# Optimization experiments

Hardware: AMD Instinct MI355X
Metric: run time of the kernel (lower is better)

The kernel has to match this reference:

```python
import jax, jax.numpy as jnp
import numpy as np

B, Q, K, D = 8, 2048, 2048, 512

def setup_inputs() -> dict:
    key = jax.random.key(0)
    k1, k2, k3, k4, k5 = jax.random.split(key, 5)
    return {
        "query": jax.random.normal(k1, (B, Q, D), dtype=jnp.float32),
        "key": jax.random.normal(k2, (B, K, D), dtype=jnp.float32),
        "value": jax.random.normal(k3, (B, K, D), dtype=jnp.float32),
        "key_mask": jax.random.randint(k4, (B, K), 0, 2, dtype=jnp.int32),
        "W": jax.random.normal(k5, (D, D), dtype=jnp.float32) / np.sqrt(D),
    }

def reference(query, key, value, key_mask, W):
    # bilinear score: s[b,q,k] = query[b,q,:] @ W @ key[b,k,:]
    scale = 1.0 / jnp.sqrt(jnp.asarray(query.shape[-1], query.dtype))
    qW = jnp.einsum('bqd,de->bqe', query, W)          # [B,Q,D]
    scores = jnp.einsum('bqe,bke->bqk', qW, key)      # [B,Q,K]
    scores = jnp.where(key_mask[:, None, :] == 0, jnp.asarray(-1e20, scores.dtype), scores) * scale
    dist = jax.nn.softmax(scores, axis=-1)            # [B,Q,K]
    context = jnp.einsum('bqk,bkd->bqd', dist, value) # [B,Q,D]
    return context, dist
```

## Files before the change

### kernel.cpp

```cpp
#include <hip/hip_runtime.h>
#include <stdint.h>

#define BB 8
#define QQ 2048
#define KK 2048
#define DD 512

typedef _Float16 f16x8 __attribute__((ext_vector_type(8)));
typedef float f32x4 __attribute__((ext_vector_type(4)));

__device__ __forceinline__ unsigned short f2h(float f) {
    union { _Float16 h; unsigned short u; } x;
    x.h = (_Float16)f;
    return x.u;
}
__device__ __forceinline__ float h2f(unsigned short u) {
    union { unsigned short u; _Float16 h; } x;
    x.u = u;
    return (float)x.h;
}

__device__ __forceinline__ void async16(const unsigned short* g, unsigned short* l) {
    __builtin_amdgcn_global_load_lds(
        (const __attribute__((address_space(1))) unsigned int*)g,
        (__attribute__((address_space(3))) unsigned int*)l, 16, 0, 0);
}

__global__ __launch_bounds__(256) void cvt_f32_f16_2(const float* __restrict__ in0,
                                                     const float* __restrict__ in1,
                                                     unsigned short* __restrict__ out0,
                                                     unsigned short* __restrict__ out1) {
    const float* in = blockIdx.y ? in1 : in0;
    unsigned short* out = blockIdx.y ? out1 : out0;
    size_t i = ((size_t)blockIdx.x * 256 + threadIdx.x) * 8;
    float4 a = *(const float4*)(in + i);
    float4 b = *(const float4*)(in + i + 4);
    uint4 u;
    u.x = (unsigned)f2h(a.x) | ((unsigned)f2h(a.y) << 16);
    u.y = (unsigned)f2h(a.z) | ((unsigned)f2h(a.w) << 16);
    u.z = (unsigned)f2h(b.x) | ((unsigned)f2h(b.y) << 16);
    u.w = (unsigned)f2h(b.z) | ((unsigned)f2h(b.w) << 16);
    *(uint4*)(out + i) = u;
}

__global__ __launch_bounds__(256) void transpose_cvt(const float* __restrict__ in,
                                                     unsigned short* __restrict__ out,
                                                     int R, int C, long inB, long outB) {
    __shared__ float t[32][33];
    const float* ip = in + (size_t)blockIdx.z * inB;
    unsigned short* op = out + (size_t)blockIdx.z * outB;
    int x = threadIdx.x & 31, y0 = threadIdx.x >> 5;
    int c0 = blockIdx.x * 32, r0 = blockIdx.y * 32;
#pragma unroll
    for (int i = 0; i < 32; i += 8)
        t[y0 + i][x] = ip[(size_t)(r0 + y0 + i) * C + c0 + x];
    __syncthreads();
#pragma unroll
    for (int i = 0; i < 32; i += 8)
        op[(size_t)(c0 + y0 + i) * R + r0 + x] = f2h(t[x][y0 + i]);
}

template <int OUTM>
__global__ __launch_bounds__(512, 2) void gemm256n(
    const unsigned short* __restrict__ Aall, const unsigned short* __restrict__ Ball,
    void* __restrict__ Call, const float* __restrict__ sums,
    int Kred, int lda, int ldb, int ldc,
    long aStride, long bStride, long cStride) {
    const int gx = gridDim.x, gy = gridDim.y;
    const int nwg = gx * gy * (int)gridDim.z;
    const int p = ((int)blockIdx.z * gy + (int)blockIdx.y) * gx + (int)blockIdx.x;
    const int qch = nwg >> 3, rch = nwg & 7;
    const int xcd = p & 7, ooff = p >> 3;
    const int w = (xcd < rch ? xcd * (qch + 1) : rch * (qch + 1) + (xcd - rch) * qch) + ooff;
    const int b = w / (gx * gy);
    const int rem = w - b * (gx * gy);
    const int my = rem / gx;
    const int nx = rem - my * gx;
    const int m0 = my * 256;
    const int n0 = nx * 128;

    __shared__ unsigned short As[4][256 * 32];
    __shared__ unsigned short Bs[4][128 * 32];

    const int tid = threadIdx.x;
    const int lane = tid & 63, wv = tid >> 6;
    const int wm = wv >> 2, wn = wv & 3;
    const int lrow = lane & 15, quad = lane >> 4;

    const int sr = lane >> 2;
    const int ssl = (lane & 3) ^ ((sr >> 1) & 3);
    const unsigned short* Ab = Aall + (size_t)b * aStride + (size_t)m0 * lda;
    const unsigned short* Bb = Ball + (size_t)b * bStride + (size_t)n0 * ldb;

    const int NT = Kred >> 5;

    auto stageA = [&](int t) {
#pragma unroll
        for (int j = 0; j < 2; j++) {
            const int c = wv * 2 + j;
            const int r = c * 16 + sr;
            async16(Ab + (size_t)r * lda + t * 32 + ssl * 8, &As[t & 3][c * 512]);
        }
    };
    auto stageB = [&](int t) {
        const int c = wv;
        const int r = c * 16 + sr;
        async16(Bb + (size_t)r * ldb + t * 32 + ssl * 8, &Bs[t & 3][c * 512]);
    };

    f32x4 acc[8][2];
#pragma unroll
    for (int mi = 0; mi < 8; mi++)
#pragma unroll
        for (int ni = 0; ni < 2; ni++)
            acc[mi][ni] = (f32x4){0.f, 0.f, 0.f, 0.f};

    for (int tt = 0; tt < 3 && tt < NT; ++tt) { stageA(tt); stageB(tt); }

    const int rsw = (lrow >> 1) & 3;

    for (int t = 0; t < NT; ++t) {
        if (t + 2 < NT)      asm volatile("s_waitcnt vmcnt(6)" ::: "memory");
        else if (t + 1 < NT) asm volatile("s_waitcnt vmcnt(3)" ::: "memory");
        else                 asm volatile("s_waitcnt vmcnt(0)" ::: "memory");
        __builtin_amdgcn_s_barrier();
        __builtin_amdgcn_sched_barrier(0);

        const unsigned short* Asl = As[t & 3];
        const unsigned short* Bsl = Bs[t & 3];
        f16x8 af[4], bfr[2];

        if (t + 3 < NT) stageA(t + 3);
#pragma unroll
        for (int ni = 0; ni < 2; ni++)
            bfr[ni] = *(const f16x8*)&Bsl[(wn * 32 + ni * 16 + lrow) * 32 + ((quad ^ rsw) * 8)];
#pragma unroll
        for (int mi = 0; mi < 4; mi++)
            af[mi] = *(const f16x8*)&Asl[(wm * 128 + mi * 16 + lrow) * 32 + ((quad ^ rsw) * 8)];
        __builtin_amdgcn_s_setprio(1);
#pragma unroll
        for (int mi = 0; mi < 4; mi++)
#pragma unroll
            for (int ni = 0; ni < 2; ni++)
                acc[mi][ni] = __builtin_amdgcn_mfma_f32_16x16x32_f16(af[mi], bfr[ni],
                                                                     acc[mi][ni], 0, 0, 0);
        __builtin_amdgcn_s_setprio(0);

        if (t + 3 < NT) stageB(t + 3);
#pragma unroll
        for (int mi = 0; mi < 4; mi++)
            af[mi] = *(const f16x8*)&Asl[(wm * 128 + (mi + 4) * 16 + lrow) * 32 + ((quad ^ rsw) * 8)];
        __builtin_amdgcn_s_setprio(1);
#pragma unroll
        for (int mi = 0; mi < 4; mi++)
#pragma unroll
            for (int ni = 0; ni < 2; ni++)
                acc[mi + 4][ni] = __builtin_amdgcn_mfma_f32_16x16x32_f16(af[mi], bfr[ni],
                                                                         acc[mi + 4][ni], 0, 0, 0);
        __builtin_amdgcn_s_setprio(0);
    }

#pragma unroll
    for (int mi = 0; mi < 8; mi++) {
        const int gm = m0 + wm * 128 + mi * 16 + quad * 4;
        if constexpr (OUTM == 0) {
            unsigned short* C = (unsigned short*)Call + (size_t)b * cStride;
#pragma unroll
            for (int ni = 0; ni < 2; ni++) {
                int gn = n0 + wn * 32 + ni * 16 + lrow;
#pragma unroll
                for (int r = 0; r < 4; r++)
                    C[(size_t)(gm + r) * ldc + gn] = f2h(acc[mi][ni][r]);
            }
        } else {
            float* C = (float*)Call + (size_t)b * cStride;
            const float* s = sums + (size_t)b * QQ;
            float iv[4];
#pragma unroll
            for (int r = 0; r < 4; r++) iv[r] = 1.0f / s[gm + r];
#pragma unroll
            for (int ni = 0; ni < 2; ni++) {
                int gn = n0 + wn * 32 + ni * 16 + lrow;
#pragma unroll
                for (int r = 0; r < 4; r++)
                    C[(size_t)(gm + r) * ldc + gn] = acc[mi][ni][r] * iv[r];
            }
        }
    }
}

__global__ __launch_bounds__(512, 2) void gemm256_exp(
    const unsigned short* __restrict__ Aall, const unsigned short* __restrict__ Ball,
    unsigned short* __restrict__ Call, const int* __restrict__ maskAll,
    float* __restrict__ sums, int Kred, int lda, int ldb, int ldc,
    long aStride, long bStride, long cStride, int maskStride, float scale) {
    const int gx = gridDim.x, gy = gridDim.y;
    const int nwg = gx * gy * (int)gridDim.z;
    const int p = ((int)blockIdx.z * gy + (int)blockIdx.y) * gx + (int)blockIdx.x;
    const int qch = nwg >> 3, rch = nwg & 7;
    const int xcd = p & 7, ooff = p >> 3;
    const int w = (xcd < rch ? xcd * (qch + 1) : rch * (qch + 1) + (xcd - rch) * qch) + ooff;
    const int b = w / (gx * gy);
    const int rem = w - b * (gx * gy);
    const int my = rem / gx;
    const int nx = rem - my * gx;
    const int m0 = my * 256;
    const int n0 = nx * 256;

    __shared__ unsigned short As[4][256 * 32];
    __shared__ unsigned short Bs[4][256 * 32];

    const int tid = threadIdx.x;
    const int lane = tid & 63, wv = tid >> 6;
    const int wm = wv >> 2, wn = wv & 3;
    const int lrow = lane & 15, quad = lane >> 4;

    const int sr = lane >> 2;
    const int ssl = (lane & 3) ^ ((sr >> 1) & 3);
    const unsigned short* Ab = Aall + (size_t)b * aStride + (size_t)m0 * lda;
    const unsigned short* Bb = Ball + (size_t)b * bStride + (size_t)n0 * ldb;

    const int NT = Kred >> 5;

    auto stageA = [&](int t) {
#pragma unroll
        for (int j = 0; j < 2; j++) {
            const int c = wv * 2 + j;
            const int r = c * 16 + sr;
            async16(Ab + (size_t)r * lda + t * 32 + ssl * 8, &As[t & 3][c * 512]);
        }
    };
    auto stageB = [&](int t) {
#pragma unroll
        for (int j = 0; j < 2; j++) {
            const int c = wv * 2 + j;
            const int r = c * 16 + sr;
            async16(Bb + (size_t)r * ldb + t * 32 + ssl * 8, &Bs[t & 3][c * 512]);
        }
    };

    f32x4 acc[8][4];
#pragma unroll
    for (int mi = 0; mi < 8; mi++)
#pragma unroll
        for (int ni = 0; ni < 4; ni++)
            acc[mi][ni] = (f32x4){0.f, 0.f, 0.f, 0.f};

    for (int tt = 0; tt < 3 && tt < NT; ++tt) { stageA(tt); stageB(tt); }

    const int rsw = (lrow >> 1) & 3;

    for (int t = 0; t < NT; ++t) {
        if (t + 2 < NT)      asm volatile("s_waitcnt vmcnt(8)" ::: "memory");
        else if (t + 1 < NT) asm volatile("s_waitcnt vmcnt(4)" ::: "memory");
        else                 asm volatile("s_waitcnt vmcnt(0)" ::: "memory");
        __builtin_amdgcn_s_barrier();
        __builtin_amdgcn_sched_barrier(0);

        const unsigned short* Asl = As[t & 3];
        const unsigned short* Bsl = Bs[t & 3];
        f16x8 af[4], bfr[4];

        if (t + 3 < NT) stageA(t + 3);
#pragma unroll
        for (int ni = 0; ni < 4; ni++)
            bfr[ni] = *(const f16x8*)&Bsl[(wn * 64 + ni * 16 + lrow) * 32 + ((quad ^ rsw) * 8)];
#pragma unroll
        for (int mi = 0; mi < 4; mi++)
            af[mi] = *(const f16x8*)&Asl[(wm * 128 + mi * 16 + lrow) * 32 + ((quad ^ rsw) * 8)];
        __builtin_amdgcn_s_setprio(1);
#pragma unroll
        for (int mi = 0; mi < 4; mi++)
#pragma unroll
            for (int ni = 0; ni < 4; ni++)
                acc[mi][ni] = __builtin_amdgcn_mfma_f32_16x16x32_f16(af[mi], bfr[ni],
                                                                     acc[mi][ni], 0, 0, 0);
        __builtin_amdgcn_s_setprio(0);

        if (t + 3 < NT) stageB(t + 3);
#pragma unroll
        for (int mi = 0; mi < 4; mi++)
            af[mi] = *(const f16x8*)&Asl[(wm * 128 + (mi + 4) * 16 + lrow) * 32 + ((quad ^ rsw) * 8)];
        __builtin_amdgcn_s_setprio(1);
#pragma unroll
        for (int mi = 0; mi < 4; mi++)
#pragma unroll
            for (int ni = 0; ni < 4; ni++)
                acc[mi + 4][ni] = __builtin_amdgcn_mfma_f32_16x16x32_f16(af[mi], bfr[ni],
                                                                         acc[mi + 4][ni], 0, 0, 0);
        __builtin_amdgcn_s_setprio(0);
    }

    unsigned short* C = Call + (size_t)b * cStride;
    const int* mk = maskAll + (size_t)b * maskStride;
#pragma unroll
    for (int mi = 0; mi < 8; mi++) {
        const int gm = m0 + wm * 128 + mi * 16 + quad * 4;
        float ps[4] = {0.f, 0.f, 0.f, 0.f};
#pragma unroll
        for (int ni = 0; ni < 4; ni++) {
            int gn = n0 + wn * 64 + ni * 16 + lrow;
            bool keep = mk[gn] != 0;
#pragma unroll
            for (int r = 0; r < 4; r++) {
                float e = keep ? __expf(acc[mi][ni][r] * scale) : 0.f;
                C[(size_t)(gm + r) * ldc + gn] = f2h(e);
                ps[r] += e;
            }
        }
#pragma unroll
        for (int off = 1; off < 16; off <<= 1)
#pragma unroll
            for (int r = 0; r < 4; r++) ps[r] += __shfl_xor(ps[r], off);
        if (lrow == 0) {
            float* s = sums + (size_t)b * QQ;
#pragma unroll
            for (int r = 0; r < 4; r++) atomicAdd(&s[gm + r], ps[r]);
        }
    }
}

__global__ __launch_bounds__(256) void normalize_rows(const unsigned short* __restrict__ expS,
                                                      const float* __restrict__ sums,
                                                      float* __restrict__ dist) {
    const unsigned short* sp = expS + (size_t)blockIdx.x * 2048;
    float* dp = dist + (size_t)blockIdx.x * 2048;
    const float inv = 1.0f / sums[blockIdx.x];
    int tid = threadIdx.x;

    uint4 u = *(const uint4*)(sp + tid * 8);
    float4 o0, o1;
    o0.x = h2f((unsigned short)(u.x & 0xffff)) * inv;
    o0.y = h2f((unsigned short)(u.x >> 16)) * inv;
    o0.z = h2f((unsigned short)(u.y & 0xffff)) * inv;
    o0.w = h2f((unsigned short)(u.y >> 16)) * inv;
    o1.x = h2f((unsigned short)(u.z & 0xffff)) * inv;
    o1.y = h2f((unsigned short)(u.z >> 16)) * inv;
    o1.z = h2f((unsigned short)(u.w & 0xffff)) * inv;
    o1.w = h2f((unsigned short)(u.w >> 16)) * inv;
    *(float4*)(dp + tid * 8) = o0;
    *(float4*)(dp + tid * 8 + 4) = o1;
}

extern "C" void kernel_launch(void* const* d_in, const int* in_sizes, int n_in,
                              void* d_out, int out_size, void* d_ws, size_t ws_size,
                              hipStream_t stream) {
    const float* q    = (const float*)d_in[0];
    const float* k    = (const float*)d_in[1];
    const float* v    = (const float*)d_in[2];
    const int*   mask = (const int*)d_in[3];
    const float* W    = (const float*)d_in[4];

    float* ctx  = (float*)d_out;
    float* dist = ctx + (size_t)BB * QQ * DD;

    unsigned short* ws  = (unsigned short*)d_ws;
    unsigned short* Wt  = ws;
    unsigned short* Qh  = Wt + (size_t)DD * DD;
    unsigned short* Kh  = Qh + (size_t)BB * QQ * DD;
    unsigned short* Vt  = Kh + (size_t)BB * KK * DD;
    unsigned short* qWh = Vt + (size_t)BB * DD * KK;
    unsigned short* Sc  = qWh + (size_t)BB * QQ * DD;
    float* sums = (float*)(Sc + (size_t)BB * QQ * KK);

    const float scale = 0.044194173824159216f;

    (void)hipMemsetAsync(sums, 0, (size_t)BB * QQ * sizeof(float), stream);
    transpose_cvt<<<dim3(DD / 32, DD / 32, 1), 256, 0, stream>>>(W, Wt, DD, DD, 0, 0);
    cvt_f32_f16_2<<<dim3((BB * QQ * DD / 8) / 256, 2), 256, 0, stream>>>(q, k, Qh, Kh);
    transpose_cvt<<<dim3(DD / 32, KK / 32, BB), 256, 0, stream>>>(
        v, Vt, KK, DD, (long)KK * DD, (long)DD * KK);
    gemm256n<0><<<dim3(DD / 128, QQ / 256, BB), 512, 0, stream>>>(
        Qh, Wt, qWh, nullptr, DD, DD, DD, DD,
        (long)QQ * DD, 0, (long)QQ * DD);
    gemm256_exp<<<dim3(KK / 256, QQ / 256, BB), 512, 0, stream>>>(
        qWh, Kh, Sc, mask, sums, DD, DD, DD, KK,
        (long)QQ * DD, (long)KK * DD, (long)QQ * KK, KK, scale);
    normalize_rows<<<dim3(BB * QQ), 256, 0, stream>>>(Sc, sums, dist);
    gemm256n<2><<<dim3(DD / 128, QQ / 256, BB), 512, 0, stream>>>(
        Sc, Vt, ctx, sums, KK, KK, KK, DD,
        (long)QQ * KK, (long)DD * KK, (long)QQ * DD);
}
```

Before: 418.9 us.

## Shrink GEMM tiles to 128x128 with three-stage LDS pipeline

```diff
diff --git a/kernel.cpp b/kernel.cpp
--- a/kernel.cpp
+++ b/kernel.cpp
@@ -61,7 +61,7 @@
 }
 
 template <int OUTM>
-__global__ __launch_bounds__(512, 2) void gemm256n(
+__global__ __launch_bounds__(512) void gemm128p(
     const unsigned short* __restrict__ Aall, const unsigned short* __restrict__ Ball,
     void* __restrict__ Call, const float* __restrict__ sums,
     int Kred, int lda, int ldb, int ldc,
@@ -76,11 +76,11 @@
     const int rem = w - b * (gx * gy);
     const int my = rem / gx;
     const int nx = rem - my * gx;
-    const int m0 = my * 256;
+    const int m0 = my * 128;
     const int n0 = nx * 128;
 
-    __shared__ unsigned short As[4][256 * 32];
-    __shared__ unsigned short Bs[4][128 * 32];
+    __shared__ unsigned short As[3][128 * 32];
+    __shared__ unsigned short Bs[3][128 * 32];
 
     const int tid = threadIdx.x;
     const int lane = tid & 63, wv = tid >> 6;
@@ -94,49 +94,44 @@
 
     const int NT = Kred >> 5;
 
-    auto stageA = [&](int t) {
-#pragma unroll
-        for (int j = 0; j < 2; j++) {
-            const int c = wv * 2 + j;
-            const int r = c * 16 + sr;
-            async16(Ab + (size_t)r * lda + t * 32 + ssl * 8, &As[t & 3][c * 512]);
-        }
+    auto stage = [&](int t, int slot) {
+        const int r = wv * 16 + sr;
+        async16(Ab + (size_t)r * lda + t * 32 + ssl * 8, &As[slot][wv * 512]);
+        async16(Bb + (size_t)r * ldb + t * 32 + ssl * 8, &Bs[slot][wv * 512]);
     };
-    auto stageB = [&](int t) {
-        const int c = wv;
-        const int r = c * 16 + sr;
-        async16(Bb + (size_t)r * ldb + t * 32 + ssl * 8, &Bs[t & 3][c * 512]);
-    };
-
-    f32x4 acc[8][2];
-#pragma unroll
-    for (int mi = 0; mi < 8; mi++)
+
+    f32x4 acc[4][2];
+#pragma unroll
+    for (int mi = 0; mi < 4; mi++)
 #pragma unroll
         for (int ni = 0; ni < 2; ni++)
             acc[mi][ni] = (f32x4){0.f, 0.f, 0.f, 0.f};
 
-    for (int tt = 0; tt < 3 && tt < NT; ++tt) { stageA(tt); stageB(tt); }
+    stage(0, 0);
+    if (NT > 1) stage(1, 1);
 
     const int rsw = (lrow >> 1) & 3;
+    int sl = 0, slp = 2;
 
     for (int t = 0; t < NT; ++t) {
-        if (t + 2 < NT)      asm volatile("s_waitcnt vmcnt(6)" ::: "memory");
-        else if (t + 1 < NT) asm volatile("s_waitcnt vmcnt(3)" ::: "memory");
-        else                 asm volatile("s_waitcnt vmcnt(0)" ::: "memory");
+        if (t + 1 < NT) asm volatile("s_waitcnt vmcnt(2)" ::: "memory");
+        else            asm volatile("s_waitcnt vmcnt(0)" ::: "memory");
         __builtin_amdgcn_s_barrier();
         __builtin_amdgcn_sched_barrier(0);
 
-        const unsigned short* Asl = As[t & 3];
-        const unsigned short* Bsl = Bs[t & 3];
+        const unsigned short* Asl = As[sl];
+        const unsigned short* Bsl = Bs[sl];
+
+        if (t + 2 < NT) stage(t + 2, slp);
+
         f16x8 af[4], bfr[2];
-
-        if (t + 3 < NT) stageA(t + 3);
 #pragma unroll
         for (int ni = 0; ni < 2; ni++)
             bfr[ni] = *(const f16x8*)&Bsl[(wn * 32 + ni * 16 + lrow) * 32 + ((quad ^ rsw) * 8)];
 #pragma unroll
         for (int mi = 0; mi < 4; mi++)
-            af[mi] = *(const f16x8*)&Asl[(wm * 128 + mi * 16 + lrow) * 32 + ((quad ^ rsw) * 8)];
+            af[mi] = *(const f16x8*)&Asl[(wm * 64 + mi * 16 + lrow) * 32 + ((quad ^ rsw) * 8)];
+
         __builtin_amdgcn_s_setprio(1);
 #pragma unroll
         for (int mi = 0; mi < 4; mi++)
@@ -146,23 +141,13 @@
                                                                      acc[mi][ni], 0, 0, 0);
         __builtin_amdgcn_s_setprio(0);
 
-        if (t + 3 < NT) stageB(t + 3);
-#pragma unroll
-        for (int mi = 0; mi < 4; mi++)
-            af[mi] = *(const f16x8*)&Asl[(wm * 128 + (mi + 4) * 16 + lrow) * 32 + ((quad ^ rsw) * 8)];
-        __builtin_amdgcn_s_setprio(1);
-#pragma unroll
-        for (int mi = 0; mi < 4; mi++)
-#pragma unroll
-            for (int ni = 0; ni < 2; ni++)
-                acc[mi + 4][ni] = __builtin_amdgcn_mfma_f32_16x16x32_f16(af[mi], bfr[ni],
-                                                                         acc[mi + 4][ni], 0, 0, 0);
-        __builtin_amdgcn_s_setprio(0);
+        sl = (sl == 2) ? 0 : sl + 1;
+        slp = (slp == 2) ? 0 : slp + 1;
     }
 
 #pragma unroll
-    for (int mi = 0; mi < 8; mi++) {
-        const int gm = m0 + wm * 128 + mi * 16 + quad * 4;
+    for (int mi = 0; mi < 4; mi++) {
+        const int gm = m0 + wm * 64 + mi * 16 + quad * 4;
         if constexpr (OUTM == 0) {
             unsigned short* C = (unsigned short*)Call + (size_t)b * cStride;
 #pragma unroll
@@ -370,14 +355,14 @@
     cvt_f32_f16_2<<<dim3((BB * QQ * DD / 8) / 256, 2), 256, 0, stream>>>(q, k, Qh, Kh);
     transpose_cvt<<<dim3(DD / 32, KK / 32, BB), 256, 0, stream>>>(
         v, Vt, KK, DD, (long)KK * DD, (long)DD * KK);
-    gemm256n<0><<<dim3(DD / 128, QQ / 256, BB), 512, 0, stream>>>(
+    gemm128p<0><<<dim3(DD / 128, QQ / 128, BB), 512, 0, stream>>>(
         Qh, Wt, qWh, nullptr, DD, DD, DD, DD,
         (long)QQ * DD, 0, (long)QQ * DD);
     gemm256_exp<<<dim3(KK / 256, QQ / 256, BB), 512, 0, stream>>>(
         qWh, Kh, Sc, mask, sums, DD, DD, DD, KK,
         (long)QQ * DD, (long)KK * DD, (long)QQ * KK, KK, scale);
     normalize_rows<<<dim3(BB * QQ), 256, 0, stream>>>(Sc, sums, dist);
-    gemm256n<2><<<dim3(DD / 128, QQ / 256, BB), 512, 0, stream>>>(
+    gemm128p<2><<<dim3(DD / 128, QQ / 128, BB), 512, 0, stream>>>(
         Sc, Vt, ctx, sums, KK, KK, KK, DD,
         (long)QQ * KK, (long)DD * KK, (long)QQ * DD);
 }
```

Result: faster. 400.6 us (-4.4%).
